# Kernel tuning notes

Measured on AMD Instinct MI355X. Metric: run time of the kernel, lower is better.

Reference implementation:

```python
import jax, jax.numpy as jnp
import numpy as np
from jax import lax

N, M, K = 192, 192, 3
B, H, W = 16, 16, 16
MK = M * K


def _deconv(x, w, b):
    # PyTorch ConvTranspose2d(k=5, stride=2, padding=2, output_padding=1)
    # == dilated conv with flipped kernel, pads (k-1-p, k-1-p+op) = (2, 3)
    wt = jnp.flip(w, (2, 3)).transpose(1, 0, 2, 3)  # (in,out,kh,kw) -> (out,in,kh,kw)
    y = lax.conv_general_dilated(x, wt, (1, 1), [(2, 3), (2, 3)],
                                 lhs_dilation=(2, 2),
                                 dimension_numbers=('NCHW', 'OIHW', 'NCHW'))
    return y + b[None, :, None, None]


def _conv(x, w, b, pad):
    y = lax.conv_general_dilated(x, w, (1, 1), [(pad, pad), (pad, pad)],
                                 dimension_numbers=('NCHW', 'OIHW', 'NCHW'))
    return y + b[None, :, None, None]


def _leaky(x):
    return jnp.where(x >= 0, x, 0.01 * x)


def setup_inputs() -> dict:
    key = jax.random.key(0)
    ks = jax.random.split(key, 19)
    s = 0.02
    d = {
        'z1': jax.random.normal(ks[0], (B, N, H, W), jnp.float32),
        # gmm_sigma branch
        'gs_w1': jax.random.normal(ks[1], (N, N, 5, 5), jnp.float32) * s,
        'gs_b1': jnp.zeros((N,), jnp.float32),
        'gs_w2': jax.random.normal(ks[2], (N, N, 5, 5), jnp.float32) * s,
        'gs_b2': jnp.zeros((N,), jnp.float32),
        'gs_w3': jax.random.normal(ks[3], (MK, N, 5, 5), jnp.float32) * s,
        'gs_b3': jnp.zeros((MK,), jnp.float32),
        # gmm_means branch
        'gm_w1': jax.random.normal(ks[4], (N, N, 5, 5), jnp.float32) * s,
        'gm_b1': jnp.zeros((N,), jnp.float32),
        'gm_w2': jax.random.normal(ks[5], (N, N, 5, 5), jnp.float32) * s,
        'gm_b2': jnp.zeros((N,), jnp.float32),
        'gm_w3': jax.random.normal(ks[6], (MK, N, 5, 5), jnp.float32) * s,
        'gm_b3': jnp.zeros((MK,), jnp.float32),
        # gmm_weights branch
        'gw_w1': jax.random.normal(ks[7], (N, N, 5, 5), jnp.float32) * s,
        'gw_b1': jnp.zeros((N,), jnp.float32),
        'gw_w2': jax.random.normal(ks[8], (N, MK, 5, 5), jnp.float32) * s,
        'gw_b2': jnp.zeros((MK,), jnp.float32),
        'gw_w3': jax.random.normal(ks[9], (MK, MK, 1, 1), jnp.float32) * s,
        'gw_b3': jnp.zeros((MK,), jnp.float32),
    }
    return d


def reference(z1, gs_w1, gs_b1, gs_w2, gs_b2, gs_w3, gs_b3,
              gm_w1, gm_b1, gm_w2, gm_b2, gm_w3, gm_b3,
              gw_w1, gw_b1, gw_w2, gw_b2, gw_w3, gw_b3):
    # sigma: deconv, ReLU, deconv, ReLU, conv(k5,s1), ReLU
    s = jax.nn.relu(_deconv(z1, gs_w1, gs_b1))
    s = jax.nn.relu(_deconv(s, gs_w2, gs_b2))
    sigma = jax.nn.relu(_conv(s, gs_w3, gs_b3, 2))
    # means: deconv, LeakyReLU, deconv, LeakyReLU, conv(k5,s1)
    m = _leaky(_deconv(z1, gm_w1, gm_b1))
    m = _leaky(_deconv(m, gm_w2, gm_b2))
    means = _conv(m, gm_w3, gm_b3, 2)
    # weights: deconv, LeakyReLU, deconv, global-max-pool, LeakyReLU, conv1x1
    w = _leaky(_deconv(z1, gw_w1, gw_b1))
    w = _deconv(w, gw_w2, gw_b2)
    w = jnp.max(w, axis=(2, 3), keepdims=True)  # fused replacement of the B*C python loop
    w = _leaky(w)
    w = _conv(w, gw_w3, gw_b3, 0)  # (B, M*K, 1, 1)
    temp = w.reshape(-1, K, M, 1, 1)
    temp = jax.nn.softmax(temp, axis=1)  # softmax over the K mixture components
    weights = temp.reshape(-1, MK, 1, 1)
    return (sigma, means, weights)
```

## Files before the change

kernel.cpp:

```cpp
#include <hip/hip_runtime.h>
#include <hip/hip_bf16.h>
#include <math.h>

typedef __attribute__((ext_vector_type(8))) short bf16x8;
typedef __attribute__((ext_vector_type(4))) float f32x4;
typedef __attribute__((ext_vector_type(16))) float f32x16;
typedef __attribute__((ext_vector_type(4))) unsigned short ushort4v;

constexpr int Bsz = 16;

__device__ __forceinline__ float act_r(float v, int a) {
  if (a == 1) return v > 0.f ? v : 0.f;
  if (a == 2) return v >= 0.f ? v : 0.01f * v;
  return v;
}

__device__ __forceinline__ unsigned short f2bf(float x) {
  __hip_bfloat16 h = __float2bfloat16(x);
  return __builtin_bit_cast(unsigned short, h);
}

__device__ __forceinline__ void gll16(const unsigned short* g, unsigned short* l) {
  __builtin_amdgcn_global_load_lds(
      (const __attribute__((address_space(1))) unsigned int*)g,
      (__attribute__((address_space(3))) unsigned int*)l, 16, 0, 0);
}

__global__ __launch_bounds__(256) void zprep_k(
    const float* __restrict__ z, unsigned short* __restrict__ zh)
{
  const int g = blockIdx.x * 256 + threadIdx.x;
  if (g >= 16 * 192 * 256) return;
  const int b  = g / 49152;
  const int rr = g - b * 49152;
  const int px = rr / 192;
  const int ic = rr - px * 192;
  const int o = ((b * 6 + (ic >> 5)) * 256 + px) * 32 + (ic & 31);
  zh[o] = f2bf(z[(b * 192 + ic) * 256 + px]);
}

__device__ __forceinline__ void dprep_one(
    const float* __restrict__ w, unsigned short* __restrict__ wh, int OC, int g)
{
  const int oc  = g % OC;
  const int rem = g / OC;
  const int icb = rem % 24;
  const int j   = rem / 24;
  bf16x8 hv;
  #pragma unroll
  for (int e = 0; e < 8; ++e)
    hv[e] = (short)f2bf(w[((icb * 8 + e) * OC + oc) * 25 + j]);
  *(bf16x8*)&wh[((j * 24 + icb) * OC + oc) * 8] = hv;
}

__global__ __launch_bounds__(256) void wprep1_k(
    const float* __restrict__ s0, const float* __restrict__ s1,
    const float* __restrict__ s2, unsigned short* __restrict__ wh)
{
  const int bid = blockIdx.x;
  const int seg = bid / 450;
  const int g   = (bid - seg * 450) * 256 + threadIdx.x;
  if (g >= 192 * 24 * 25) return;
  const float* src = seg == 0 ? s0 : (seg == 1 ? s1 : s2);
  dprep_one(src, wh + (size_t)seg * 921600, 192, g);
}

__global__ __launch_bounds__(256) void wprep_d_k(
    const float* __restrict__ w, unsigned short* __restrict__ wh, int OC)
{
  const int g = blockIdx.x * 256 + threadIdx.x;
  if (g >= OC * 24 * 25) return;
  dprep_one(w, wh, OC, g);
}

__global__ __launch_bounds__(256) void wprep_t_k(
    const float* __restrict__ w, unsigned short* __restrict__ wh)
{
  const int g = blockIdx.x * 256 + threadIdx.x;
  if (g >= 345600) return;
  const int ln = g & 15;
  int r = g >> 4;
  const int lg  = r & 3;  r >>= 2;
  const int of  = r & 3;  r >>= 2;
  const int ocb = r % 9;  r /= 9;
  const int c   = r % 6;  r /= 6;
  const int j   = r;
  const int oc  = ocb * 64 + of * 16 + ln;
  const int icb = c * 4 + lg;
  bf16x8 hv;
  #pragma unroll
  for (int e = 0; e < 8; ++e)
    hv[e] = (short)f2bf(w[oc * 4800 + (icb * 8 + e) * 25 + j]);
  *(bf16x8*)&wh[(size_t)g * 8] = hv;
}

template<int H, int OMODE, int OL, int RPW>
__global__ __launch_bounds__(256, 2) void deconv2_k(
    const unsigned short* __restrict__ xh, long x_brs,
    const unsigned short* __restrict__ wh, long w_brs,
    const float* __restrict__ b0, const float* __restrict__ b1,
    const float* __restrict__ b2,
    unsigned short* __restrict__ yh, long y_brs,
    float* __restrict__ mvp, int OC, int a0, int a1, int a2)
{
  constexpr int NF = H / 16;
  constexpr int R  = 4 * RPW;
  constexpr int PC = (H == 16) ? 20 : 36;
  __shared__ __align__(16) unsigned short xs[R + 2][4][PC][8];
  __shared__ float red[4][32];

  const int zz = blockIdx.z;
  const int br = zz >> 4;
  const int b  = zz & 15;
  const int by = blockIdx.y;
  const int r0 = by * R;
  const int oc0 = blockIdx.x * 32;
  const int t  = threadIdx.x;
  const int wv = t >> 6;
  const int l  = t & 63;
  const int lg = l >> 4;
  const int ln = l & 15;

  const unsigned short* xhp = xh + (long)br * x_brs;
  const unsigned short* whp = wh + (long)br * w_brs;
  const float* bias = br == 0 ? b0 : (br == 1 ? b1 : b2);
  const int act = br == 0 ? a0 : (br == 1 ? a1 : a2);

  f32x4 acc[RPW][4][2][NF];
  #pragma unroll
  for (int rr = 0; rr < RPW; ++rr)
    #pragma unroll
    for (int p = 0; p < 4; ++p)
      #pragma unroll
      for (int of = 0; of < 2; ++of)
        #pragma unroll
        for (int nf = 0; nf < NF; ++nf)
          acc[rr][p][of][nf] = (f32x4){0.f, 0.f, 0.f, 0.f};

  int evv[3], odv[2];
  {
    const int ev0[3] = {0, 2, 4};
    const int od0[2] = {1, 3};
    const int er = wv % 3, orr = wv & 1;
    #pragma unroll
    for (int i = 0; i < 3; ++i) { int ii = i + er; if (ii >= 3) ii -= 3; evv[i] = ev0[ii]; }
    #pragma unroll
    for (int i = 0; i < 2; ++i) { int ii = i + orr; if (ii >= 2) ii -= 2; odv[i] = od0[ii]; }
  }

  {
    unsigned short* fx = (unsigned short*)xs;
    constexpr int ZL = (R + 2) * 4 * PC;
    const bf16x8 z8 = {0,0,0,0,0,0,0,0};
    #pragma unroll
    for (int k = 0; k < (ZL + 255) / 256; ++k) {
      const int li = t + k * 256;
      if (li < ZL) *(bf16x8*)&fx[li * 8] = z8;
    }
  }

  for (int c = 0; c < 6; ++c) {
    __syncthreads();
    constexpr int DC = (R + 2) * H * 4;
    #pragma unroll
    for (int k = 0; k < (DC + 255) / 256; ++k) {
      const int li = t + k * 256;
      if (li < DC) {
        const int part = li & 3;
        const int col  = (li >> 2) & (H - 1);
        const int row  = li / (4 * H);
        const int y    = r0 - 1 + row;
        if ((unsigned)y < (unsigned)H) {
          const bf16x8 v = *(const bf16x8*)&xhp[
              (((size_t)(b * 6 + c) * H + y) * H + col) * 32 + part * 8];
          *(bf16x8*)&xs[row][part][col + 1][0] = v;
        }
      }
    }
    __syncthreads();

    #define TAP_BODY(KY2, DY, P, KX)                                        \
      {                                                                     \
        const int jT = (KY2) * 5 + (KX);                                    \
        const int dxT = 1 - ((KX) >> 1);                                    \
        bf16x8 ahT[2];                                                      \
        const int wbaseT = ((jT * 24 + c * 4 + lg) * OC + oc0 + ln) * 8;    \
        _Pragma("unroll")                                                   \
        for (int of = 0; of < 2; ++of)                                      \
          ahT[of] = *(const bf16x8*)&whp[wbaseT + of * 128];                \
        _Pragma("unroll")                                                   \
        for (int rr = 0; rr < RPW; ++rr) {                                  \
          const int rlT = RPW * wv + rr + 1 + (DY);                         \
          bf16x8 bhT[NF];                                                   \
          _Pragma("unroll")                                                 \
          for (int nf = 0; nf < NF; ++nf)                                   \
            bhT[nf] = *(const bf16x8*)&xs[rlT][lg][1 + nf * 16 + ln + dxT][0]; \
          __builtin_amdgcn_s_setprio(1);                                    \
          _Pragma("unroll")                                                 \
          for (int of = 0; of < 2; ++of)                                    \
            _Pragma("unroll")                                               \
            for (int nf = 0; nf < NF; ++nf)                                 \
              acc[rr][P][of][nf] = __builtin_amdgcn_mfma_f32_16x16x32_bf16( \
                  ahT[of], bhT[nf], acc[rr][P][of][nf], 0, 0, 0);           \
          __builtin_amdgcn_s_setprio(0);                                    \
        }                                                                   \
      }

    #pragma unroll
    for (int ki = 0; ki < 3; ++ki) {
      const int ky2 = evv[ki];
      const int dy  = 1 - (ky2 >> 1);
      #pragma unroll
      for (int kx = 0; kx < 5; ++kx)
        TAP_BODY(ky2, dy, (kx & 1), kx)
    }
    #pragma unroll
    for (int ki = 0; ki < 2; ++ki) {
      const int ky2 = odv[ki];
      const int dy  = 1 - (ky2 >> 1);
      #pragma unroll
      for (int kx = 0; kx < 5; ++kx)
        TAP_BODY(ky2, dy, (2 + (kx & 1)), kx)
    }
    #undef TAP_BODY
  }

  if (OMODE == 1) {
    const int OCG = OC >> 5;
    float bv[2][4];
    #pragma unroll
    for (int of = 0; of < 2; ++of)
      #pragma unroll
      for (int r = 0; r < 4; ++r)
        bv[of][r] = bias[oc0 + of * 16 + lg * 4 + r];
    unsigned short* yhp = yh + (long)br * y_brs;
    #pragma unroll
    for (int rr = 0; rr < RPW; ++rr) {
      const int iy = r0 + RPW * wv + rr;
      #pragma unroll
      for (int sy = 0; sy < 2; ++sy)
        #pragma unroll
        for (int sx = 0; sx < 2; ++sx) {
          const int p  = sy * 2 + sx;
          const int oy = 2 * iy + sy;
          #pragma unroll
          for (int of = 0; of < 2; ++of) {
            const int ocb = oc0 + of * 16 + lg * 4;
            const int cg  = ocb >> 5;
            const int co  = ocb & 31;
            #pragma unroll
            for (int nf = 0; nf < NF; ++nf) {
              const int ox = 2 * (nf * 16 + ln) + sx;
              ushort4v hv;
              #pragma unroll
              for (int r = 0; r < 4; ++r)
                hv[r] = f2bf(act_r(acc[rr][p][of][nf][r] + bv[of][r], act));
              size_t idx;
              if (OL) {
                const int qg = cg * 4 + (co >> 3);
                idx = (((size_t)(b * (OC >> 3) + qg) * (4 * H * H)) +
                       (size_t)oy * (2 * H) + ox) * 8 + (co & 7);
              } else {
                idx = (((size_t)(b * OCG + cg) * (4 * H * H)) +
                       (size_t)oy * (2 * H) + ox) * 32 + co;
              }
              *(ushort4v*)&yhp[idx] = hv;
            }
          }
        }
    }
  } else {
    #pragma unroll
    for (int of = 0; of < 2; ++of)
      #pragma unroll
      for (int r = 0; r < 4; ++r) {
        float m = -3.402823466e38f;
        #pragma unroll
        for (int rr = 0; rr < RPW; ++rr)
          #pragma unroll
          for (int p = 0; p < 4; ++p)
            #pragma unroll
            for (int nf = 0; nf < NF; ++nf)
              m = fmaxf(m, acc[rr][p][of][nf][r]);
        #pragma unroll
        for (int off = 1; off < 16; off <<= 1)
          m = fmaxf(m, __shfl_xor(m, off));
        if (ln == 0)
          red[wv][of * 16 + lg * 4 + r] = m + bias[oc0 + of * 16 + lg * 4 + r];
      }
    __syncthreads();
    if (t < 32) {
      const float v = fmaxf(fmaxf(red[0][t], red[1][t]), fmaxf(red[2][t], red[3][t]));
      mvp[((b * 4) + by) * OC + oc0 + t] = v;
    }
  }
}

__global__ __launch_bounds__(256, 3) void conv3_k(
    const unsigned short* __restrict__ gxh,
    const unsigned short* __restrict__ gwh,
    const float* __restrict__ bias, float* __restrict__ out, int act)
{
  __shared__ __align__(16) unsigned short xs[8][4][80][8];

  const int bid  = blockIdx.x;
  const int orig = (bid & 7) * 288 + (bid >> 3);
  const int ocg  = orig >> 8;
  const int rem  = orig & 255;
  const int b    = rem >> 4;
  const int band = rem & 15;
  const int y0   = band * 4;
  const int oc0  = ocg * 64;
  const int t    = threadIdx.x;
  const int wv   = t >> 6;
  const int l    = t & 63;
  const int lg   = l >> 4;
  const int ln   = l & 15;

  f32x4 acc[4][4];
  #pragma unroll
  for (int of = 0; of < 4; ++of)
    #pragma unroll
    for (int pf = 0; pf < 4; ++pf)
      acc[of][pf] = (f32x4){0.f, 0.f, 0.f, 0.f};

  int ky2v[5], rlv[5];
  #pragma unroll
  for (int ky = 0; ky < 5; ++ky) {
    int k2 = ky + wv; if (k2 >= 5) k2 -= 5;
    ky2v[ky] = k2; rlv[ky] = wv + k2;
  }

  {
    unsigned short* fx = (unsigned short*)xs;
    const bf16x8 z8 = {0,0,0,0,0,0,0,0};
    #pragma unroll
    for (int k = 0; k < 10; ++k) {
      const int li = t + k * 256;
      if (li < 2560) *(bf16x8*)&fx[li * 8] = z8;
    }
  }

  for (int c = 0; c < 6; ++c) {
    __syncthreads();
    #pragma unroll
    for (int k = 0; k < 8; ++k) {
      const int idx = k * 4 + wv;
      const int row = idx >> 2, q = idx & 3;
      const int y = y0 - 2 + row;
      if ((unsigned)y < 64u) {
        const unsigned short* g = &gxh[
            ((((size_t)b * 24 + c * 4 + q) << 12) + ((size_t)y << 6) + l) * 8];
        gll16(g, &xs[row][q][2][0]);
      }
    }
    __syncthreads();

    const unsigned short* wrow =
        gwh + (size_t)c * 18432 + (size_t)ocg * 2048 + (size_t)l * 8;
    const unsigned short* xrow[5];
    #pragma unroll
    for (int ky = 0; ky < 5; ++ky)
      xrow[ky] = &xs[rlv[ky]][lg][ln][0];

    bf16x8 ah[2][4], bx[2][4];

    #define LDW(KY, KX, S)                                                  \
      {                                                                     \
        const unsigned short* wj = wrow + (size_t)(ky2v[KY] * 5 + (KX)) * 110592; \
        _Pragma("unroll")                                                   \
        for (int of = 0; of < 4; ++of)                                      \
          ah[S][of] = *(const bf16x8*)&wj[of * 512];                        \
        const unsigned short* xr = xrow[KY];                                \
        _Pragma("unroll")                                                   \
        for (int pf = 0; pf < 4; ++pf)                                      \
          bx[S][pf] = *(const bf16x8*)&xr[(pf * 16 + (KX)) * 8];            \
      }

    LDW(0, 0, 0)
    #pragma unroll
    for (int j = 0; j < 25; ++j) {
      const int s = j & 1;
      if (j < 24) {
        const int jn = j + 1;
        const int kyn = jn / 5, kxn = jn % 5;
        const int ns = jn & 1;
        LDW(kyn, kxn, ns)
      }
      __builtin_amdgcn_sched_barrier(0);
      __builtin_amdgcn_s_setprio(1);
      #pragma unroll
      for (int of = 0; of < 4; ++of)
        #pragma unroll
        for (int pf = 0; pf < 4; ++pf)
          acc[of][pf] = __builtin_amdgcn_mfma_f32_16x16x32_bf16(
              ah[s][of], bx[s][pf], acc[of][pf], 0, 0, 0);
      __builtin_amdgcn_s_setprio(0);
    }
    #undef LDW
  }

  const int y = y0 + wv;
  #pragma unroll
  for (int of = 0; of < 4; ++of)
    #pragma unroll
    for (int r = 0; r < 4; ++r) {
      const int oc = oc0 + of * 16 + lg * 4 + r;
      const float bv = bias[oc];
      float* po = &out[(((size_t)(b * 576 + oc) * 64) + y) * 64 + ln];
      #pragma unroll
      for (int pf = 0; pf < 4; ++pf)
        po[16 * pf] = act_r(acc[of][pf][r] + bv, act);
    }
}

__global__ __launch_bounds__(256) void head_k(
    const float* __restrict__ mvp, const float* __restrict__ w3,
    const float* __restrict__ b3, float* __restrict__ outw)
{
  __shared__ float lv[576];
  __shared__ float yv[576];
  const int b = blockIdx.x;
  const int t = threadIdx.x;
  for (int i = t; i < 576; i += 256) {
    float m = mvp[(b * 4 + 0) * 576 + i];
    #pragma unroll
    for (int ti = 1; ti < 4; ++ti)
      m = fmaxf(m, mvp[(b * 4 + ti) * 576 + i]);
    lv[i] = m >= 0.f ? m : 0.01f * m;
  }
  __syncthreads();
  for (int oc = t; oc < 576; oc += 256) {
    float s = b3[oc];
    for (int c = 0; c < 576; ++c) s += w3[oc * 576 + c] * lv[c];
    yv[oc] = s;
  }
  __syncthreads();
  if (t < 192) {
    const float v0 = yv[t], v1 = yv[192 + t], v2 = yv[384 + t];
    const float mx = fmaxf(v0, fmaxf(v1, v2));
    const float e0 = expf(v0 - mx), e1 = expf(v1 - mx), e2 = expf(v2 - mx);
    const float inv = 1.f / (e0 + e1 + e2);
    outw[b * 576 + t]       = e0 * inv;
    outw[b * 576 + 192 + t] = e1 * inv;
    outw[b * 576 + 384 + t] = e2 * inv;
  }
}

extern "C" void kernel_launch(void* const* d_in, const int* in_sizes, int n_in,
                              void* d_out, int out_size, void* d_ws, size_t ws_size,
                              hipStream_t stream)
{
  (void)in_sizes; (void)n_in; (void)out_size; (void)ws_size;

  const float* z1    = (const float*)d_in[0];
  const float* gs_w1 = (const float*)d_in[1];
  const float* gs_b1 = (const float*)d_in[2];
  const float* gs_w2 = (const float*)d_in[3];
  const float* gs_b2 = (const float*)d_in[4];
  const float* gs_w3 = (const float*)d_in[5];
  const float* gs_b3 = (const float*)d_in[6];
  const float* gm_w1 = (const float*)d_in[7];
  const float* gm_b1 = (const float*)d_in[8];
  const float* gm_w2 = (const float*)d_in[9];
  const float* gm_b2 = (const float*)d_in[10];
  const float* gm_w3 = (const float*)d_in[11];
  const float* gm_b3 = (const float*)d_in[12];
  const float* gw_w1 = (const float*)d_in[13];
  const float* gw_b1 = (const float*)d_in[14];
  const float* gw_w2 = (const float*)d_in[15];
  const float* gw_b2 = (const float*)d_in[16];
  const float* gw_w3 = (const float*)d_in[17];
  const float* gw_b3 = (const float*)d_in[18];

  unsigned short* p = (unsigned short*)d_ws;
  unsigned short* Z   = p; p += 786432;
  unsigned short* A1  = p; p += (size_t)3 * 3145728;
  unsigned short* A2  = p; p += 12582912;
  unsigned short* W1  = p; p += (size_t)3 * 921600;
  unsigned short* Wb  = p; p += 2764800;
  float* MVp = (float*)p;

  float* o_sigma = (float*)d_out;
  float* o_means = o_sigma + (size_t)Bsz * 576 * 64 * 64;
  float* o_w     = o_means + (size_t)Bsz * 576 * 64 * 64;

  dim3 blk(256);

  zprep_k<<<dim3(3072), blk, 0, stream>>>(z1, Z);
  wprep1_k<<<dim3(1350), blk, 0, stream>>>(gs_w1, gm_w1, gw_w1, W1);

  deconv2_k<16,1,0,2><<<dim3(6,2,48), blk, 0, stream>>>(
      Z, 0, W1, 921600, gs_b1, gm_b1, gw_b1,
      A1, 3145728, nullptr, 192, 1, 2, 2);

  wprep_d_k<<<dim3(450), blk, 0, stream>>>(gs_w2, Wb, 192);
  deconv2_k<32,1,1,2><<<dim3(6,4,16), blk, 0, stream>>>(
      A1, 0, Wb, 0, gs_b2, gs_b2, gs_b2,
      A2, 0, nullptr, 192, 1, 1, 1);
  wprep_t_k<<<dim3(1350), blk, 0, stream>>>(gs_w3, Wb);
  conv3_k<<<dim3(2304), blk, 0, stream>>>(A2, Wb, gs_b3, o_sigma, 1);

  wprep_d_k<<<dim3(450), blk, 0, stream>>>(gm_w2, Wb, 192);
  deconv2_k<32,1,1,2><<<dim3(6,4,16), blk, 0, stream>>>(
      A1 + (size_t)3145728, 0, Wb, 0, gm_b2, gm_b2, gm_b2,
      A2, 0, nullptr, 192, 2, 2, 2);
  wprep_t_k<<<dim3(1350), blk, 0, stream>>>(gm_w3, Wb);
  conv3_k<<<dim3(2304), blk, 0, stream>>>(A2, Wb, gm_b3, o_means, 0);

  wprep_d_k<<<dim3(1350), blk, 0, stream>>>(gw_w2, Wb, 576);
  deconv2_k<32,2,0,2><<<dim3(18,4,16), blk, 0, stream>>>(
      A1 + (size_t)2 * 3145728, 0, Wb, 0,
      gw_b2, gw_b2, gw_b2, nullptr, 0, MVp, 576, 0, 0, 0);
  head_k<<<dim3(16), blk, 0, stream>>>(MVp, gw_w3, gw_b3, o_w);
}
```

Measured before the change: 1.001 ms.

## Batch sigma and means branches into merged deconv2 and conv3 launches

Adds a workspace-size-gated path that keeps separate activation and weight buffers for the sigma and means branches. Their second deconvolutions and their final 5x5 convolutions can then each run as one launch with a branch grid dimension, instead of two serialized launches. This targets launch tails and low occupancy between back-to-back kernels, at the cost of a larger workspace. If the workspace is too small, the original sequential path is used.

```diff
diff --git a/kernel.cpp b/kernel.cpp
--- a/kernel.cpp
+++ b/kernel.cpp
@@ -297,11 +297,20 @@
 }
 
 __global__ __launch_bounds__(256, 3) void conv3_k(
-    const unsigned short* __restrict__ gxh,
-    const unsigned short* __restrict__ gwh,
-    const float* __restrict__ bias, float* __restrict__ out, int act)
+    const unsigned short* __restrict__ gxh, long x_brs,
+    const unsigned short* __restrict__ gwh, long w_brs,
+    const float* __restrict__ bias0, const float* __restrict__ bias1,
+    float* __restrict__ out0, float* __restrict__ out1,
+    int act0, int act1)
 {
   __shared__ __align__(16) unsigned short xs[8][4][80][8];
+
+  const int brz  = blockIdx.y;
+  const unsigned short* gx = gxh + (long)brz * x_brs;
+  const unsigned short* gw = gwh + (long)brz * w_brs;
+  const float* bias = brz ? bias1 : bias0;
+  float* out = brz ? out1 : out0;
+  const int act = brz ? act1 : act0;
 
   const int bid  = blockIdx.x;
   const int orig = (bid & 7) * 288 + (bid >> 3);
@@ -349,7 +358,7 @@
       const int row = idx >> 2, q = idx & 3;
       const int y = y0 - 2 + row;
       if ((unsigned)y < 64u) {
-        const unsigned short* g = &gxh[
+        const unsigned short* g = &gx[
             ((((size_t)b * 24 + c * 4 + q) << 12) + ((size_t)y << 6) + l) * 8];
         gll16(g, &xs[row][q][2][0]);
       }
@@ -357,7 +366,7 @@
     __syncthreads();
 
     const unsigned short* wrow =
-        gwh + (size_t)c * 18432 + (size_t)ocg * 2048 + (size_t)l * 8;
+        gw + (size_t)c * 18432 + (size_t)ocg * 2048 + (size_t)l * 8;
     const unsigned short* xrow[5];
     #pragma unroll
     for (int ky = 0; ky < 5; ++ky)
@@ -451,7 +460,7 @@
                               void* d_out, int out_size, void* d_ws, size_t ws_size,
                               hipStream_t stream)
 {
-  (void)in_sizes; (void)n_in; (void)out_size; (void)ws_size;
+  (void)in_sizes; (void)n_in; (void)out_size;
 
   const float* z1    = (const float*)d_in[0];
   const float* gs_w1 = (const float*)d_in[1];
@@ -473,44 +482,83 @@
   const float* gw_w3 = (const float*)d_in[17];
   const float* gw_b3 = (const float*)d_in[18];
 
-  unsigned short* p = (unsigned short*)d_ws;
-  unsigned short* Z   = p; p += 786432;
-  unsigned short* A1  = p; p += (size_t)3 * 3145728;
-  unsigned short* A2  = p; p += 12582912;
-  unsigned short* W1  = p; p += (size_t)3 * 921600;
-  unsigned short* Wb  = p; p += 2764800;
-  float* MVp = (float*)p;
-
   float* o_sigma = (float*)d_out;
   float* o_means = o_sigma + (size_t)Bsz * 576 * 64 * 64;
   float* o_w     = o_means + (size_t)Bsz * 576 * 64 * 64;
 
   dim3 blk(256);
 
-  zprep_k<<<dim3(3072), blk, 0, stream>>>(z1, Z);
-  wprep1_k<<<dim3(1350), blk, 0, stream>>>(gs_w1, gm_w1, gw_w1, W1);
-
-  deconv2_k<16,1,0,2><<<dim3(6,2,48), blk, 0, stream>>>(
-      Z, 0, W1, 921600, gs_b1, gm_b1, gw_b1,
-      A1, 3145728, nullptr, 192, 1, 2, 2);
-
-  wprep_d_k<<<dim3(450), blk, 0, stream>>>(gs_w2, Wb, 192);
-  deconv2_k<32,1,1,2><<<dim3(6,4,16), blk, 0, stream>>>(
-      A1, 0, Wb, 0, gs_b2, gs_b2, gs_b2,
-      A2, 0, nullptr, 192, 1, 1, 1);
-  wprep_t_k<<<dim3(1350), blk, 0, stream>>>(gs_w3, Wb);
-  conv3_k<<<dim3(2304), blk, 0, stream>>>(A2, Wb, gs_b3, o_sigma, 1);
-
-  wprep_d_k<<<dim3(450), blk, 0, stream>>>(gm_w2, Wb, 192);
-  deconv2_k<32,1,1,2><<<dim3(6,4,16), blk, 0, stream>>>(
-      A1 + (size_t)3145728, 0, Wb, 0, gm_b2, gm_b2, gm_b2,
-      A2, 0, nullptr, 192, 2, 2, 2);
-  wprep_t_k<<<dim3(1350), blk, 0, stream>>>(gm_w3, Wb);
-  conv3_k<<<dim3(2304), blk, 0, stream>>>(A2, Wb, gm_b3, o_means, 0);
-
-  wprep_d_k<<<dim3(1350), blk, 0, stream>>>(gw_w2, Wb, 576);
-  deconv2_k<32,2,0,2><<<dim3(18,4,16), blk, 0, stream>>>(
-      A1 + (size_t)2 * 3145728, 0, Wb, 0,
-      gw_b2, gw_b2, gw_b2, nullptr, 0, MVp, 576, 0, 0, 0);
-  head_k<<<dim3(16), blk, 0, stream>>>(MVp, gw_w3, gw_b3, o_w);
-}
+  const size_t NEED_MERGED = 87515136;
+  const bool merged = ws_size >= NEED_MERGED;
+
+  if (merged) {
+    unsigned short* p = (unsigned short*)d_ws;
+    unsigned short* Z   = p; p += 786432;
+    unsigned short* A1  = p; p += (size_t)3 * 3145728;
+    unsigned short* A2  = p; p += (size_t)2 * 12582912;
+    unsigned short* Wd  = p; p += 2764800;
+    unsigned short* Wt  = p; p += (size_t)2 * 2764800;
+    float* MVp = (float*)p;
+
+    zprep_k<<<dim3(3072), blk, 0, stream>>>(z1, Z);
+    wprep1_k<<<dim3(1350), blk, 0, stream>>>(gs_w1, gm_w1, gw_w1, Wd);
+
+    deconv2_k<16,1,0,2><<<dim3(6,2,48), blk, 0, stream>>>(
+        Z, 0, Wd, 921600, gs_b1, gm_b1, gw_b1,
+        A1, 3145728, nullptr, 192, 1, 2, 2);
+
+    wprep_d_k<<<dim3(450), blk, 0, stream>>>(gs_w2, Wd, 192);
+    wprep_d_k<<<dim3(450), blk, 0, stream>>>(gm_w2, Wd + 921600, 192);
+    deconv2_k<32,1,1,2><<<dim3(6,4,32), blk, 0, stream>>>(
+        A1, 3145728, Wd, 921600, gs_b2, gm_b2, gm_b2,
+        A2, 12582912, nullptr, 192, 1, 2, 2);
+
+    wprep_t_k<<<dim3(1350), blk, 0, stream>>>(gs_w3, Wt);
+    wprep_t_k<<<dim3(1350), blk, 0, stream>>>(gm_w3, Wt + 2764800);
+    conv3_k<<<dim3(2304, 2), blk, 0, stream>>>(
+        A2, 12582912, Wt, 2764800, gs_b3, gm_b3, o_sigma, o_means, 1, 0);
+
+    wprep_d_k<<<dim3(1350), blk, 0, stream>>>(gw_w2, Wd, 576);
+    deconv2_k<32,2,0,2><<<dim3(18,4,16), blk, 0, stream>>>(
+        A1 + (size_t)2 * 3145728, 0, Wd, 0,
+        gw_b2, gw_b2, gw_b2, nullptr, 0, MVp, 576, 0, 0, 0);
+    head_k<<<dim3(16), blk, 0, stream>>>(MVp, gw_w3, gw_b3, o_w);
+  } else {
+    unsigned short* p = (unsigned short*)d_ws;
+    unsigned short* Z   = p; p += 786432;
+    unsigned short* A1  = p; p += (size_t)3 * 3145728;
+    unsigned short* A2  = p; p += 12582912;
+    unsigned short* W1  = p; p += (size_t)3 * 921600;
+    unsigned short* Wb  = p; p += 2764800;
+    float* MVp = (float*)p;
+
+    zprep_k<<<dim3(3072), blk, 0, stream>>>(z1, Z);
+    wprep1_k<<<dim3(1350), blk, 0, stream>>>(gs_w1, gm_w1, gw_w1, W1);
+
+    deconv2_k<16,1,0,2><<<dim3(6,2,48), blk, 0, stream>>>(
+        Z, 0, W1, 921600, gs_b1, gm_b1, gw_b1,
+        A1, 3145728, nullptr, 192, 1, 2, 2);
+
+    wprep_d_k<<<dim3(450), blk, 0, stream>>>(gs_w2, Wb, 192);
+    deconv2_k<32,1,1,2><<<dim3(6,4,16), blk, 0, stream>>>(
+        A1, 0, Wb, 0, gs_b2, gs_b2, gs_b2,
+        A2, 0, nullptr, 192, 1, 1, 1);
+    wprep_t_k<<<dim3(1350), blk, 0, stream>>>(gs_w3, Wb);
+    conv3_k<<<dim3(2304, 1), blk, 0, stream>>>(
+        A2, 0, Wb, 0, gs_b3, gs_b3, o_sigma, o_sigma, 1, 1);
+
+    wprep_d_k<<<dim3(450), blk, 0, stream>>>(gm_w2, Wb, 192);
+    deconv2_k<32,1,1,2><<<dim3(6,4,16), blk, 0, stream>>>(
+        A1 + (size_t)3145728, 0, Wb, 0, gm_b2, gm_b2, gm_b2,
+        A2, 0, nullptr, 192, 2, 2, 2);
+    wprep_t_k<<<dim3(1350), blk, 0, stream>>>(gm_w3, Wb);
+    conv3_k<<<dim3(2304, 1), blk, 0, stream>>>(
+        A2, 0, Wb, 0, gm_b3, gm_b3, o_means, o_means, 0, 0);
+
+    wprep_d_k<<<dim3(1350), blk, 0, stream>>>(gw_w2, Wb, 576);
+    deconv2_k<32,2,0,2><<<dim3(18,4,16), blk, 0, stream>>>(
+        A1 + (size_t)2 * 3145728, 0, Wb, 0,
+        gw_b2, gw_b2, gw_b2, nullptr, 0, MVp, 576, 0, 0, 0);
+    head_k<<<dim3(16), blk, 0, stream>>>(MVp, gw_w3, gw_b3, o_w);
+  }
+}
```

Result: no change. 988.7 us (-1.2%).
